# Optimization experiments

Hardware: AMD Instinct MI355X
Metric: run time of the kernel (lower is better)

The kernel has to match this reference:

```python
import jax, jax.numpy as jnp
import numpy as np
from jax.ops import segment_sum, segment_max

N = 400000          # points
V = 100000          # occupied voxels
EPS = 1e-3          # BN eps from norm_cfg
VX, VY, VZ = 0.2, 0.2, 4.0          # voxel_size
X0, Y0, Z0 = 0.0, -40.0, -3.0       # point_cloud_range mins
GX, GY, GZ = 352, 400, 1            # grid dims


def setup_inputs() -> dict:
    key = jax.random.key(0)
    ks = jax.random.split(key, 12)
    # points: xyz uniform inside the point cloud range, 4th channel = intensity
    xyz = jax.random.uniform(ks[0], (N, 3), jnp.float32) \
        * jnp.array([70.4, 80.0, 4.0], jnp.float32) \
        + jnp.array([X0, Y0, Z0], jnp.float32)
    inten = jax.random.uniform(ks[1], (N, 1), jnp.float32)
    features = jnp.concatenate([xyz, inten], axis=1)
    # point -> voxel mapping; guarantee every voxel id occupied so
    # segment_max semantics match torch's unique-voxel reduce exactly
    inv = jnp.concatenate([jnp.arange(V, dtype=jnp.int32),
                           jax.random.randint(ks[2], (N - V,), 0, V, jnp.int32)])
    inv = jax.random.permutation(ks[3], inv)
    # voxel coordinates (batch, z, y, x)
    b = jax.random.randint(ks[4], (V,), 0, 2, jnp.int32)
    z = jnp.zeros((V,), jnp.int32)
    y = jax.random.randint(ks[5], (V,), 0, GY, jnp.int32)
    x = jax.random.randint(ks[6], (V,), 0, GX, jnp.int32)
    coors = jnp.stack([b, z, y, x], axis=1)
    # VFE params: Linear(bias=False) + BN1d(gamma, beta)
    W0 = jax.random.normal(ks[7], (64, 10), jnp.float32) * (1.0 / np.sqrt(10))
    W1 = jax.random.normal(ks[8], (64, 128), jnp.float32) * (1.0 / np.sqrt(128))
    return dict(features=features, W0=W0,
                gamma0=jnp.ones((64,), jnp.float32), beta0=jnp.zeros((64,), jnp.float32),
                W1=W1,
                gamma1=jnp.ones((64,), jnp.float32), beta1=jnp.zeros((64,), jnp.float32),
                inv=inv, coors=coors)


def _bn_relu(x, gamma, beta):
    # BN1d in training mode: biased batch stats over the point dim
    mu = jnp.mean(x, axis=0)
    var = jnp.var(x, axis=0)
    return jax.nn.relu(gamma * (x - mu) * jax.lax.rsqrt(var + EPS) + beta)


def _stats(xyz, inv, coors):
    # cluster-center offset: per-voxel mean of xyz, gathered back
    cnt = segment_sum(jnp.ones((xyz.shape[0],), xyz.dtype), inv, num_segments=V)
    mean = segment_sum(xyz, inv, num_segments=V) / cnt[:, None]
    f_cluster = xyz - mean[inv]
    # voxel-center offset: coors order is (batch, z, y, x)
    cf = coors.astype(xyz.dtype)
    center = jnp.stack([cf[:, 3] * VX + VX / 2 + X0,
                        cf[:, 2] * VY + VY / 2 + Y0,
                        cf[:, 1] * VZ + VZ / 2 + Z0], axis=1)
    f_center = xyz - center[inv]
    return jnp.concatenate([xyz, f_cluster, f_center], axis=1)  # [N, 9]


def reference(features, W0, gamma0, beta0, W1, gamma1, beta1, inv, coors):
    x = jnp.concatenate([_stats(features[:, :3], inv, coors), features[:, 3:]], axis=1)  # [N,10]
    # VFE layer 0
    h0 = _bn_relu(x @ W0.T, gamma0, beta0)                     # [N,64]
    v0 = segment_max(h0, inv, num_segments=V)                  # [V,64]
    x1 = jnp.concatenate([h0, v0[inv]], axis=1)                # [N,128]
    # VFE layer 1
    h1 = _bn_relu(x1 @ W1.T, gamma1, beta1)                    # [N,64]
    voxel_feats = segment_max(h1, inv, num_segments=V)         # [V,64]
    return voxel_feats, coors
```

## Files before the change

### kernel.cpp

```cpp
#include <hip/hip_runtime.h>
#include <hip/hip_bf16.h>

#define NPTS 400000
#define NVOX 100000
#define EPSB 1e-3f
#define NTILE 6250
#define NBLK_SCAN 391
#define GBLK 782

#define OFF_ACC4   0
#define OFF_GRAM   (4*NVOX)
#define OFF_STATS  (OFF_GRAM + 72)
#define OFF_P1     (OFF_STATS + 256)
#define ZERO_FLOATS (OFF_P1 + 4096)
#define OFF_V0     ZERO_FLOATS
#define OFF_Y1M    (OFF_V0 + NVOX*64)
#define OFF_VTMP   (OFF_Y1M + NVOX*64)
#define OFF_BSUM   (OFF_VTMP + NVOX)
#define OFF_VOFF   (OFF_BSUM + 512)
#define OFF_VSTART (OFF_VOFF + NVOX)
#define OFF_ORD    (OFF_VSTART + NVOX + 8)
#define OFF_VS     (OFF_ORD + NPTS)
#define OFF_W0F    (OFF_VS + NPTS)
#define OFF_W1B    (OFF_W0F + 640)
#define OFF_H0T    (OFF_W1B + 4096)

#define XTB_LD 136
#define HT_LD  65

typedef __bf16 bf16x8 __attribute__((ext_vector_type(8)));
typedef float  f32x4  __attribute__((ext_vector_type(4)));

__device__ __forceinline__ float b2f(__hip_bfloat16 h) { return __bfloat162float(h); }
__device__ __forceinline__ float bfbits2f(unsigned short u) {
    return __uint_as_float((unsigned int)u << 16);
}
__device__ __forceinline__ unsigned short bf16u(float f) {
    __hip_bfloat16 h = __float2bfloat16(f);
    return __builtin_bit_cast(unsigned short, h);
}
__device__ __forceinline__ unsigned int fkey(float f) {
    unsigned int u = __float_as_uint(f);
    return (u & 0x80000000u) ? ~u : (u | 0x80000000u);
}
__device__ __forceinline__ float funkey(unsigned int k) {
    unsigned int u = (k & 0x80000000u) ? (k & 0x7FFFFFFFu) : ~k;
    return __uint_as_float(u);
}

__device__ __forceinline__ void compute_x(const __hip_bfloat16* __restrict__ feat,
                                          const float* __restrict__ acc4,
                                          const int* __restrict__ coors,
                                          long i, int v, float* xv) {
    ushort4 f4 = *(const ushort4*)(feat + 4 * i);
    float px = bfbits2f(f4.x), py = bfbits2f(f4.y), pz = bfbits2f(f4.z), it = bfbits2f(f4.w);
    float4 a4 = *(const float4*)&acc4[4 * (long)v];
    float ic = 1.0f / a4.x;
    int4 c4 = *(const int4*)&coors[4 * (long)v];
    xv[0] = px; xv[1] = py; xv[2] = pz;
    xv[3] = px - a4.y * ic; xv[4] = py - a4.z * ic; xv[5] = pz - a4.w * ic;
    xv[6] = px - ((float)c4.w * 0.2f + 0.1f);
    xv[7] = py - ((float)c4.z * 0.2f + 0.1f - 40.0f);
    xv[8] = pz - ((float)c4.y * 4.0f + 2.0f - 3.0f);
    xv[9] = it;
}

__global__ void k_vsum(const __hip_bfloat16* __restrict__ feat,
                       const int* __restrict__ inv,
                       float* __restrict__ acc4,
                       const __hip_bfloat16* __restrict__ W0,
                       const __hip_bfloat16* __restrict__ W1,
                       float* __restrict__ W0f, unsigned short* __restrict__ w1b) {
    if (blockIdx.x == 6250) {
        int t = threadIdx.x;
        for (int j = t; j < 640; j += 256) W0f[j] = b2f(W0[j]);
        for (int f = t; f < 8192; f += 256) {
            int j  = f & 7;
            int l  = (f >> 3) & 63;
            int ks = (f >> 9) & 3;
            int ct = f >> 11;
            int ch = ct * 16 + (l & 15);
            int k  = ks * 32 + ((l >> 4) & 3) * 8 + j;
            w1b[f] = __builtin_bit_cast(unsigned short, W1[ch * 128 + k]);
        }
        return;
    }
    long t = (long)blockIdx.x * 256 + threadIdx.x;
    int pt = (int)(t >> 2);
    int comp = (int)(t & 3);
    float val = (comp == 0) ? 1.0f : b2f(feat[4 * pt + comp - 1]);
    int v = inv[pt];
    atomicAdd(&acc4[(long)v * 4 + comp], val);
}

__global__ void k_scan1(const float* __restrict__ acc4,
                        int* __restrict__ vtmp, int* __restrict__ bsum) {
    __shared__ int sc[256];
    int b = blockIdx.x, t = threadIdx.x;
    int v = b * 256 + t;
    int c = (v < NVOX) ? (int)acc4[4 * (long)v] : 0;
    sc[t] = c;
    __syncthreads();
    int val = c;
    for (int off = 1; off < 256; off <<= 1) {
        int x = (t >= off) ? sc[t - off] : 0;
        __syncthreads();
        val += x; sc[t] = val;
        __syncthreads();
    }
    if (v < NVOX) vtmp[v] = val - c;
    if (t == 255) bsum[b] = val;
}

__global__ void k_scan2(int* __restrict__ bsum) {
    __shared__ int sc[512];
    int t = threadIdx.x;
    int c = (t < NBLK_SCAN) ? bsum[t] : 0;
    sc[t] = c;
    __syncthreads();
    int val = c;
    for (int off = 1; off < 512; off <<= 1) {
        int x = (t >= off) ? sc[t - off] : 0;
        __syncthreads();
        val += x; sc[t] = val;
        __syncthreads();
    }
    if (t < NBLK_SCAN) bsum[t] = val - c;
}

__global__ void k_scan3(const int* __restrict__ vtmp, const int* __restrict__ bsum,
                        int* __restrict__ voff, int* __restrict__ vstart,
                        float* __restrict__ v0, unsigned int* __restrict__ y1m) {
    int v = blockIdx.x * 256 + threadIdx.x;
    if (v < NVOX) {
        int s0 = vtmp[v] + bsum[v >> 8];
        voff[v] = s0;
        vstart[v] = s0;
        int s1;
        if (v + 1 < NVOX) s1 = vtmp[v + 1] + bsum[(v + 1) >> 8];
        else              s1 = NPTS;
        if ((s0 >> 4) != ((s1 - 1) >> 4)) {
            float4 z4 = {0.f, 0.f, 0.f, 0.f};
            float4* pv = (float4*)&v0[(long)v * 64];
            float4* py = (float4*)&y1m[(long)v * 64];
#pragma unroll
            for (int u = 0; u < 16; u++) { pv[u] = z4; py[u] = z4; }
        }
    }
    if (v == 0) vstart[NVOX] = NPTS;
}

__global__ __launch_bounds__(256, 4)
void k_prep(const __hip_bfloat16* __restrict__ feat,
            const int* __restrict__ inv,
            const int* __restrict__ coors,
            const float* __restrict__ acc4,
            int* __restrict__ voff,
            int* __restrict__ ord, int* __restrict__ vsorted,
            float* __restrict__ gram) {
    __shared__ float gs[72];
    int t = threadIdx.x;
    if (t < 72) gs[t] = 0.0f;
    __syncthreads();

    float sx[10], sxx[55];
#pragma unroll
    for (int a = 0; a < 10; a++) sx[a] = 0.0f;
#pragma unroll
    for (int a = 0; a < 55; a++) sxx[a] = 0.0f;

    for (long i = (long)blockIdx.x * 256 + t; i < NPTS; i += (long)GBLK * 256) {
        int v = inv[i];
        float xv[10];
        compute_x(feat, acc4, coors, i, v, xv);
        int idx = 0;
#pragma unroll
        for (int a = 0; a < 10; a++) {
            sx[a] += xv[a];
#pragma unroll
            for (int b = 0; b <= a; b++) sxx[idx++] += xv[a] * xv[b];
        }
        int pos = atomicAdd(&voff[v], 1);
        ord[pos] = (int)i;
        vsorted[pos] = v;
    }

#pragma unroll
    for (int v = 0; v < 65; v++) {
        float s = (v < 10) ? sx[v] : sxx[v - 10];
        for (int m = 32; m >= 1; m >>= 1) s += __shfl_xor(s, m);
        if ((t & 63) == 0) atomicAdd(&gs[v], s);
    }
    __syncthreads();
    if (t < 65) atomicAdd(&gram[t], gs[t]);
}

__global__ __launch_bounds__(256, 8)
void k_h0max(const int* __restrict__ ord, const int* __restrict__ vsorted,
             const int* __restrict__ vstart,
             const __hip_bfloat16* __restrict__ feat,
             const float* __restrict__ acc4, const int* __restrict__ coors,
             const float* __restrict__ W0f, const float* __restrict__ gram,
             const __hip_bfloat16* __restrict__ g0,
             const __hip_bfloat16* __restrict__ be0,
             float* __restrict__ v0, unsigned short* __restrict__ h0t) {
    __shared__ float ht[64 * HT_LD];
    __shared__ int invs[64];
    __shared__ float xvs[640];
    __shared__ float sc0s[64], bi0s[64];
    int t = threadIdx.x, w = t >> 6, l = t & 63;
    int base = blockIdx.x * 64;

    if (w == 0) {
        int i = ord[base + l];
        int v = vsorted[base + l];
        invs[l] = v;
        float xv[10];
        compute_x(feat, acc4, coors, (long)i, v, xv);
#pragma unroll
        for (int k = 0; k < 10; k++) xvs[k * 64 + l] = xv[k];
    } else if (w == 1) {
        int c = l;
        float wr[10];
#pragma unroll
        for (int k = 0; k < 10; k++) wr[k] = W0f[c * 10 + k];
        float sum = 0.0f, sq = 0.0f;
#pragma unroll
        for (int a = 0; a < 10; a++) {
            sum += wr[a] * gram[a];
            float ta = 0.0f;
#pragma unroll
            for (int b = 0; b < 10; b++) {
                int hi = (a >= b) ? a : b, lo = (a >= b) ? b : a;
                ta += wr[b] * gram[10 + hi * (hi + 1) / 2 + lo];
            }
            sq += wr[a] * ta;
        }
        float mu  = sum * (1.0f / NPTS);
        float var = sq * (1.0f / NPTS) - mu * mu;
        float g   = b2f(g0[c]) * rsqrtf(var + EPSB);
        sc0s[c] = g;
        bi0s[c] = b2f(be0[c]) - mu * g;
    }
    __syncthreads();

    float xv[10];
#pragma unroll
    for (int k = 0; k < 10; k++) xv[k] = xvs[k * 64 + l];
    int cw = w * 16;
#pragma unroll
    for (int j = 0; j < 16; j++) {
        int c = cw + j;
        float y = 0.0f;
#pragma unroll
        for (int k = 0; k < 10; k++) y += xv[k] * W0f[c * 10 + k];
        ht[l * HT_LD + c] = fmaxf(sc0s[c] * y + bi0s[c], 0.0f);
    }
    __syncthreads();

#pragma unroll
    for (int u = 0; u < 2; u++) {
        int idx = t + u * 256;
        int pt2 = idx >> 3;
        int c0 = (idx & 7) * 8;
        const float* src = &ht[pt2 * HT_LD + c0];
        float4 a  = *(const float4*)src;
        float4 b4 = *(const float4*)(src + 4);
        uint4 o;
        o.x = (unsigned int)bf16u(a.x)  | ((unsigned int)bf16u(a.y)  << 16);
        o.y = (unsigned int)bf16u(a.z)  | ((unsigned int)bf16u(a.w)  << 16);
        o.z = (unsigned int)bf16u(b4.x) | ((unsigned int)bf16u(b4.y) << 16);
        o.w = (unsigned int)bf16u(b4.z) | ((unsigned int)bf16u(b4.w) << 16);
        *(uint4*)&h0t[(long)(base + pt2) * 64 + c0] = o;
    }

    unsigned int mk = 0u;
#pragma unroll
    for (int j = 0; j < 16; j++) {
        int p = cw + j;
        unsigned int hb = __float_as_uint(ht[p * HT_LD + l]);
        mk = (hb > mk) ? hb : mk;
        if (j == 15 || invs[p + 1] != invs[p]) {
            int vv = invs[p];
            int s0 = vstart[vv], s1 = vstart[vv + 1];
            unsigned int* dst = (unsigned int*)&v0[(long)vv * 64 + l];
            if (s0 >= base + cw && s1 <= base + cw + 16)
                *dst = mk;
            else
                atomicMax(dst, mk);
            mk = 0u;
        }
    }
}

__global__ __launch_bounds__(256, 8)
void k_mfma_stats(const int* __restrict__ vsorted,
                  const int* __restrict__ vstart,
                  const unsigned short* __restrict__ h0t,
                  const unsigned short* __restrict__ w1b,
                  const float* __restrict__ v0,
                  float* __restrict__ P1,
                  unsigned int* __restrict__ y1m) {
    __shared__ union {
        unsigned short xtb[64 * XTB_LD];
        float ht[64 * HT_LD];
    } sm;
    __shared__ int invs[64];
    int t = threadIdx.x, w = t >> 6, l = t & 63;
    int quad = l >> 4, lm = l & 15;
    int base = blockIdx.x * 64;
    if (w == 0) invs[l] = vsorted[base + l];

    bf16x8 bfrag[4];
    const uint4* wf = (const uint4*)w1b;
#pragma unroll
    for (int ks = 0; ks < 4; ks++)
        bfrag[ks] = __builtin_bit_cast(bf16x8, wf[(w * 4 + ks) * 64 + l]);

#pragma unroll
    for (int u = 0; u < 2; u++) {
        int idx = t + u * 256;
        int pt = idx >> 3, c0 = (idx & 7) * 8;
        uint4 d = *(const uint4*)&h0t[(long)(base + pt) * 64 + c0];
        *(uint4*)&sm.xtb[pt * XTB_LD + c0] = d;
    }
    {
        int p = t >> 2, q = t & 3;
        int vv = vsorted[base + p];
        const float4* src = (const float4*)&v0[(long)vv * 64 + q * 16];
#pragma unroll
        for (int u = 0; u < 4; u++) {
            float4 f4 = src[u];
            ushort4 s4 = { bf16u(f4.x), bf16u(f4.y), bf16u(f4.z), bf16u(f4.w) };
            *(ushort4*)&sm.xtb[p * XTB_LD + 64 + q * 16 + 4 * u] = s4;
        }
    }
    __syncthreads();

    f32x4 acc[4];
#pragma unroll
    for (int pg = 0; pg < 4; pg++) acc[pg] = (f32x4){0.f, 0.f, 0.f, 0.f};
#pragma unroll
    for (int ks = 0; ks < 4; ks++) {
#pragma unroll
        for (int pg = 0; pg < 4; pg++) {
            const uint4* ap = (const uint4*)&sm.xtb[(pg * 16 + lm) * XTB_LD + ks * 32 + quad * 8];
            bf16x8 a = __builtin_bit_cast(bf16x8, *ap);
            acc[pg] = __builtin_amdgcn_mfma_f32_16x16x32_bf16(a, bfrag[ks], acc[pg], 0, 0, 0);
        }
    }

    float ssum = 0.0f, ssq = 0.0f;
#pragma unroll
    for (int pg = 0; pg < 4; pg++) {
#pragma unroll
        for (int r = 0; r < 4; r++) {
            float y = acc[pg][r];
            ssum += y; ssq += y * y;
        }
    }
    __syncthreads();

#pragma unroll
    for (int pg = 0; pg < 4; pg++) {
#pragma unroll
        for (int r = 0; r < 4; r++)
            sm.ht[(pg * 16 + quad * 4 + r) * HT_LD + w * 16 + lm] = acc[pg][r];
    }
    __syncthreads();

    unsigned int mk = 0u;
    int cw = w * 16;
#pragma unroll
    for (int j = 0; j < 16; j++) {
        int p = cw + j;
        unsigned int k2 = fkey(sm.ht[p * HT_LD + l]);
        mk = (k2 > mk) ? k2 : mk;
        if (j == 15 || invs[p + 1] != invs[p]) {
            int vv = invs[p];
            int s0 = vstart[vv], s1 = vstart[vv + 1];
            unsigned int* dst = &y1m[(long)vv * 64 + l];
            if (s0 >= base + cw && s1 <= base + cw + 16)
                *dst = mk;
            else
                atomicMax(dst, mk);
            mk = 0u;
        }
    }

    ssum += __shfl_xor(ssum, 16); ssq += __shfl_xor(ssq, 16);
    ssum += __shfl_xor(ssum, 32); ssq += __shfl_xor(ssq, 32);
    if (l < 16) {
        int slot = blockIdx.x & 31;
        atomicAdd(&P1[slot * 128 + w * 16 + lm], ssum);
        atomicAdd(&P1[slot * 128 + 64 + w * 16 + lm], ssq);
    }
}

#define OUTBLK 512
__global__ __launch_bounds__(256)
void k_out(const unsigned int* __restrict__ y1m,
           const float* __restrict__ P1,
           const __hip_bfloat16* __restrict__ gamma,
           const __hip_bfloat16* __restrict__ beta,
           const int* __restrict__ coors,
           float* __restrict__ out) {
    __shared__ float sc1s[64], bi1s[64];
    int t = threadIdx.x;
    if (t < 64) {
        float sum = 0.0f, sq = 0.0f;
        for (int s = 0; s < 32; s++) {
            sum += P1[s*128 + t];
            sq  += P1[s*128 + 64 + t];
        }
        float mu  = sum * (1.0f / NPTS);
        float var = sq * (1.0f / NPTS) - mu * mu;
        float g   = b2f(gamma[t]) * rsqrtf(var + EPSB);
        sc1s[t] = g;
        bi1s[t] = b2f(beta[t]) - mu * g;
    }
    __syncthreads();

    const long n4feat = (long)NVOX * 16;
    const long n4all  = n4feat + NVOX;
    const long nfeat  = (long)NVOX * 64;
    for (long idx = (long)blockIdx.x * 256 + t; idx < n4all; idx += (long)OUTBLK * 256) {
        if (idx < n4feat) {
            uint4 kk = ((const uint4*)y1m)[idx];
            int c0 = (int)((idx * 4) & 63);
            float4 o;
            o.x = fmaxf(sc1s[c0+0] * funkey(kk.x) + bi1s[c0+0], 0.0f);
            o.y = fmaxf(sc1s[c0+1] * funkey(kk.y) + bi1s[c0+1], 0.0f);
            o.z = fmaxf(sc1s[c0+2] * funkey(kk.z) + bi1s[c0+2], 0.0f);
            o.w = fmaxf(sc1s[c0+3] * funkey(kk.w) + bi1s[c0+3], 0.0f);
            ((float4*)out)[idx] = o;
        } else {
            long vi = idx - n4feat;
            int4 c4 = ((const int4*)coors)[vi];
            float4 o;
            o.x = b2f(__float2bfloat16((float)c4.x));
            o.y = b2f(__float2bfloat16((float)c4.y));
            o.z = b2f(__float2bfloat16((float)c4.z));
            o.w = b2f(__float2bfloat16((float)c4.w));
            ((float4*)(out + nfeat))[vi] = o;
        }
    }
}

extern "C" void kernel_launch(void* const* d_in, const int* in_sizes, int n_in,
                              void* d_out, int out_size, void* d_ws, size_t ws_size,
                              hipStream_t stream) {
    const __hip_bfloat16* feat = (const __hip_bfloat16*)d_in[0];
    const __hip_bfloat16* W0   = (const __hip_bfloat16*)d_in[1];
    const __hip_bfloat16* g0   = (const __hip_bfloat16*)d_in[2];
    const __hip_bfloat16* be0  = (const __hip_bfloat16*)d_in[3];
    const __hip_bfloat16* W1   = (const __hip_bfloat16*)d_in[4];
    const __hip_bfloat16* g1   = (const __hip_bfloat16*)d_in[5];
    const __hip_bfloat16* be1  = (const __hip_bfloat16*)d_in[6];
    const int* inv   = (const int*)d_in[7];
    const int* coors = (const int*)d_in[8];
    float* out = (float*)d_out;

    float* ws    = (float*)d_ws;
    float* acc4  = ws + OFF_ACC4;
    float* gram  = ws + OFF_GRAM;
    float* P1    = ws + OFF_P1;
    float* v0    = ws + OFF_V0;
    unsigned int* y1m = (unsigned int*)(ws + OFF_Y1M);
    int* vtmp    = (int*)(ws + OFF_VTMP);
    int* bsum    = (int*)(ws + OFF_BSUM);
    int* voff    = (int*)(ws + OFF_VOFF);
    int* vstart  = (int*)(ws + OFF_VSTART);
    int* ord     = (int*)(ws + OFF_ORD);
    int* vsorted = (int*)(ws + OFF_VS);
    float* W0f   = ws + OFF_W0F;
    unsigned short* w1b = (unsigned short*)(ws + OFF_W1B);
    unsigned short* h0t = (unsigned short*)(ws + OFF_H0T);

    hipMemsetAsync(ws, 0, (size_t)ZERO_FLOATS * sizeof(float), stream);

    k_vsum<<<6251, 256, 0, stream>>>(feat, inv, acc4, W0, W1, W0f, w1b);
    k_scan1<<<NBLK_SCAN, 256, 0, stream>>>(acc4, vtmp, bsum);
    k_scan2<<<1, 512, 0, stream>>>(bsum);
    k_scan3<<<NBLK_SCAN, 256, 0, stream>>>(vtmp, bsum, voff, vstart, v0, y1m);
    k_prep<<<GBLK, 256, 0, stream>>>(feat, inv, coors, acc4, voff, ord, vsorted, gram);
    k_h0max<<<NTILE, 256, 0, stream>>>(ord, vsorted, vstart, feat, acc4, coors,
                                       W0f, gram, g0, be0, v0, h0t);
    k_mfma_stats<<<NTILE, 256, 0, stream>>>(vsorted, vstart, h0t, w1b, v0, P1, y1m);
    k_out<<<OUTBLK, 256, 0, stream>>>(y1m, P1, g1, be1, coors, out);
}
```

Baseline: 265.9 us.

## Fuse layer-0 VFE and layer-1 MFMA kernels, recomputing boundary voxel halos

Merges the h0/segment-max kernel and the MFMA layer-1 kernel into one. Each 64-point tile computes h0 directly into shared memory and keeps per-voxel maxima in an LDS table. For voxels that straddle the tile edge, it recomputes the neighbouring points' h0 so the v0 max is complete locally. This removes the global h0t and v0 buffers, their zeroing, and one launch, in exchange for redundant halo work, LDS atomics, and lower occupancy from a larger shared footprint.

Result: slower. 276.4 us (+3.9%).

```diff
diff --git a/kernel.cpp b/kernel.cpp
--- a/kernel.cpp
+++ b/kernel.cpp
@@ -10,11 +10,9 @@
 
 #define OFF_ACC4   0
 #define OFF_GRAM   (4*NVOX)
-#define OFF_STATS  (OFF_GRAM + 72)
-#define OFF_P1     (OFF_STATS + 256)
+#define OFF_P1     (OFF_GRAM + 128)
 #define ZERO_FLOATS (OFF_P1 + 4096)
-#define OFF_V0     ZERO_FLOATS
-#define OFF_Y1M    (OFF_V0 + NVOX*64)
+#define OFF_Y1M    ZERO_FLOATS
 #define OFF_VTMP   (OFF_Y1M + NVOX*64)
 #define OFF_BSUM   (OFF_VTMP + NVOX)
 #define OFF_VOFF   (OFF_BSUM + 512)
@@ -23,7 +21,6 @@
 #define OFF_VS     (OFF_ORD + NPTS)
 #define OFF_W0F    (OFF_VS + NPTS)
 #define OFF_W1B    (OFF_W0F + 640)
-#define OFF_H0T    (OFF_W1B + 4096)
 
 #define XTB_LD 136
 #define HT_LD  65
@@ -130,7 +127,7 @@
 
 __global__ void k_scan3(const int* __restrict__ vtmp, const int* __restrict__ bsum,
                         int* __restrict__ voff, int* __restrict__ vstart,
-                        float* __restrict__ v0, unsigned int* __restrict__ y1m) {
+                        unsigned int* __restrict__ y1m) {
     int v = blockIdx.x * 256 + threadIdx.x;
     if (v < NVOX) {
         int s0 = vtmp[v] + bsum[v >> 8];
@@ -141,10 +138,9 @@
         else              s1 = NPTS;
         if ((s0 >> 4) != ((s1 - 1) >> 4)) {
             float4 z4 = {0.f, 0.f, 0.f, 0.f};
-            float4* pv = (float4*)&v0[(long)v * 64];
             float4* py = (float4*)&y1m[(long)v * 64];
 #pragma unroll
-            for (int u = 0; u < 16; u++) { pv[u] = z4; py[u] = z4; }
+            for (int u = 0; u < 16; u++) py[u] = z4;
         }
     }
     if (v == 0) vstart[NVOX] = NPTS;
@@ -195,21 +191,35 @@
     if (t < 65) atomicAdd(&gram[t], gs[t]);
 }
 
-__global__ __launch_bounds__(256, 8)
-void k_h0max(const int* __restrict__ ord, const int* __restrict__ vsorted,
+__global__ __launch_bounds__(256, 4)
+void k_fused(const int* __restrict__ ord, const int* __restrict__ vsorted,
              const int* __restrict__ vstart,
              const __hip_bfloat16* __restrict__ feat,
              const float* __restrict__ acc4, const int* __restrict__ coors,
              const float* __restrict__ W0f, const float* __restrict__ gram,
              const __hip_bfloat16* __restrict__ g0,
              const __hip_bfloat16* __restrict__ be0,
-             float* __restrict__ v0, unsigned short* __restrict__ h0t) {
-    __shared__ float ht[64 * HT_LD];
+             const unsigned short* __restrict__ w1b,
+             float* __restrict__ P1, unsigned int* __restrict__ y1m) {
+    __shared__ union {
+        unsigned short xtb[64 * XTB_LD];
+        float ht[64 * HT_LD];
+    } sm;
+    __shared__ unsigned int vms[64 * 65];
+    __shared__ float xvs[640];
     __shared__ int invs[64];
-    __shared__ float xvs[640];
     __shared__ float sc0s[64], bi0s[64];
+    __shared__ int sext[2];
+
     int t = threadIdx.x, w = t >> 6, l = t & 63;
+    int quad = l >> 4, lm = l & 15;
     int base = blockIdx.x * 64;
+
+#pragma unroll
+    for (int u = 0; u < 17; u++) {
+        int idx = t + u * 256;
+        if (idx < 64 * 65) vms[idx] = 0u;
+    }
 
     if (w == 0) {
         int i = ord[base + l];
@@ -219,6 +229,8 @@
         compute_x(feat, acc4, coors, (long)i, v, xv);
 #pragma unroll
         for (int k = 0; k < 10; k++) xvs[k * 64 + l] = xv[k];
+        if (l == 0)  sext[0] = vstart[v];
+        if (l == 63) sext[1] = vstart[v + 1];
     } else if (w == 1) {
         int c = l;
         float wr[10];
@@ -242,74 +254,6 @@
         sc0s[c] = g;
         bi0s[c] = b2f(be0[c]) - mu * g;
     }
-    __syncthreads();
-
-    float xv[10];
-#pragma unroll
-    for (int k = 0; k < 10; k++) xv[k] = xvs[k * 64 + l];
-    int cw = w * 16;
-#pragma unroll
-    for (int j = 0; j < 16; j++) {
-        int c = cw + j;
-        float y = 0.0f;
-#pragma unroll
-        for (int k = 0; k < 10; k++) y += xv[k] * W0f[c * 10 + k];
-        ht[l * HT_LD + c] = fmaxf(sc0s[c] * y + bi0s[c], 0.0f);
-    }
-    __syncthreads();
-
-#pragma unroll
-    for (int u = 0; u < 2; u++) {
-        int idx = t + u * 256;
-        int pt2 = idx >> 3;
-        int c0 = (idx & 7) * 8;
-        const float* src = &ht[pt2 * HT_LD + c0];
-        float4 a  = *(const float4*)src;
-        float4 b4 = *(const float4*)(src + 4);
-        uint4 o;
-        o.x = (unsigned int)bf16u(a.x)  | ((unsigned int)bf16u(a.y)  << 16);
-        o.y = (unsigned int)bf16u(a.z)  | ((unsigned int)bf16u(a.w)  << 16);
-        o.z = (unsigned int)bf16u(b4.x) | ((unsigned int)bf16u(b4.y) << 16);
-        o.w = (unsigned int)bf16u(b4.z) | ((unsigned int)bf16u(b4.w) << 16);
-        *(uint4*)&h0t[(long)(base + pt2) * 64 + c0] = o;
-    }
-
-    unsigned int mk = 0u;
-#pragma unroll
-    for (int j = 0; j < 16; j++) {
-        int p = cw + j;
-        unsigned int hb = __float_as_uint(ht[p * HT_LD + l]);
-        mk = (hb > mk) ? hb : mk;
-        if (j == 15 || invs[p + 1] != invs[p]) {
-            int vv = invs[p];
-            int s0 = vstart[vv], s1 = vstart[vv + 1];
-            unsigned int* dst = (unsigned int*)&v0[(long)vv * 64 + l];
-            if (s0 >= base + cw && s1 <= base + cw + 16)
-                *dst = mk;
-            else
-                atomicMax(dst, mk);
-            mk = 0u;
-        }
-    }
-}
-
-__global__ __launch_bounds__(256, 8)
-void k_mfma_stats(const int* __restrict__ vsorted,
-                  const int* __restrict__ vstart,
-                  const unsigned short* __restrict__ h0t,
-                  const unsigned short* __restrict__ w1b,
-                  const float* __restrict__ v0,
-                  float* __restrict__ P1,
-                  unsigned int* __restrict__ y1m) {
-    __shared__ union {
-        unsigned short xtb[64 * XTB_LD];
-        float ht[64 * HT_LD];
-    } sm;
-    __shared__ int invs[64];
-    int t = threadIdx.x, w = t >> 6, l = t & 63;
-    int quad = l >> 4, lm = l & 15;
-    int base = blockIdx.x * 64;
-    if (w == 0) invs[l] = vsorted[base + l];
 
     bf16x8 bfrag[4];
     const uint4* wf = (const uint4*)w1b;
@@ -317,21 +261,75 @@
     for (int ks = 0; ks < 4; ks++)
         bfrag[ks] = __builtin_bit_cast(bf16x8, wf[(w * 4 + ks) * 64 + l]);
 
-#pragma unroll
-    for (int u = 0; u < 2; u++) {
-        int idx = t + u * 256;
-        int pt = idx >> 3, c0 = (idx & 7) * 8;
-        uint4 d = *(const uint4*)&h0t[(long)(base + pt) * 64 + c0];
-        *(uint4*)&sm.xtb[pt * XTB_LD + c0] = d;
-    }
+    __syncthreads();
+
+    int v_lo = invs[0];
+    int cw = w * 16;
+
+    {
+        float xv[10];
+#pragma unroll
+        for (int k = 0; k < 10; k++) xv[k] = xvs[k * 64 + l];
+        int slot = invs[l] - v_lo;
+#pragma unroll
+        for (int jj = 0; jj < 8; jj++) {
+            int c0 = cw + 2 * jj;
+            float ya = 0.0f, yb = 0.0f;
+#pragma unroll
+            for (int k = 0; k < 10; k++) {
+                ya += xv[k] * W0f[c0 * 10 + k];
+                yb += xv[k] * W0f[(c0 + 1) * 10 + k];
+            }
+            float ha = fmaxf(sc0s[c0] * ya + bi0s[c0], 0.0f);
+            float hb = fmaxf(sc0s[c0 + 1] * yb + bi0s[c0 + 1], 0.0f);
+            unsigned int pk = (unsigned int)bf16u(ha) | ((unsigned int)bf16u(hb) << 16);
+            *(unsigned int*)&sm.xtb[l * XTB_LD + c0] = pk;
+            atomicMax(&vms[slot * 65 + c0],     __float_as_uint(ha));
+            atomicMax(&vms[slot * 65 + c0 + 1], __float_as_uint(hb));
+        }
+    }
+
+    {
+        int s_lo = sext[0], s_hi = sext[1];
+        int L = base - s_lo;
+        int T = s_hi - (base + 64);
+        int v_hi = invs[63];
+        int slot_hi = v_hi - v_lo;
+        for (int j0 = 0; j0 < L + T; j0 += 64) {
+            int j = j0 + l;
+            if (j < L + T) {
+                int lead = (j < L) ? 1 : 0;
+                int g  = lead ? (s_lo + j) : (base + 64 + (j - L));
+                int vv = lead ? v_lo : v_hi;
+                int slot = lead ? 0 : slot_hi;
+                int i = ord[g];
+                float xv[10];
+                compute_x(feat, acc4, coors, (long)i, vv, xv);
+#pragma unroll
+                for (int jj = 0; jj < 16; jj++) {
+                    int c = cw + jj;
+                    float y = 0.0f;
+#pragma unroll
+                    for (int k = 0; k < 10; k++) y += xv[k] * W0f[c * 10 + k];
+                    float h = fmaxf(sc0s[c] * y + bi0s[c], 0.0f);
+                    atomicMax(&vms[slot * 65 + c], __float_as_uint(h));
+                }
+            }
+        }
+    }
+    __syncthreads();
+
     {
         int p = t >> 2, q = t & 3;
-        int vv = vsorted[base + p];
-        const float4* src = (const float4*)&v0[(long)vv * 64 + q * 16];
+        int slot = invs[p] - v_lo;
+        const unsigned int* src = &vms[slot * 65 + q * 16];
 #pragma unroll
         for (int u = 0; u < 4; u++) {
-            float4 f4 = src[u];
-            ushort4 s4 = { bf16u(f4.x), bf16u(f4.y), bf16u(f4.z), bf16u(f4.w) };
+            ushort4 s4;
+            s4.x = bf16u(__uint_as_float(src[4 * u + 0]));
+            s4.y = bf16u(__uint_as_float(src[4 * u + 1]));
+            s4.z = bf16u(__uint_as_float(src[4 * u + 2]));
+            s4.w = bf16u(__uint_as_float(src[4 * u + 3]));
             *(ushort4*)&sm.xtb[p * XTB_LD + 64 + q * 16 + 4 * u] = s4;
         }
     }
@@ -370,7 +368,6 @@
     __syncthreads();
 
     unsigned int mk = 0u;
-    int cw = w * 16;
 #pragma unroll
     for (int j = 0; j < 16; j++) {
         int p = cw + j;
@@ -465,7 +462,6 @@
     float* acc4  = ws + OFF_ACC4;
     float* gram  = ws + OFF_GRAM;
     float* P1    = ws + OFF_P1;
-    float* v0    = ws + OFF_V0;
     unsigned int* y1m = (unsigned int*)(ws + OFF_Y1M);
     int* vtmp    = (int*)(ws + OFF_VTMP);
     int* bsum    = (int*)(ws + OFF_BSUM);
@@ -475,17 +471,15 @@
     int* vsorted = (int*)(ws + OFF_VS);
     float* W0f   = ws + OFF_W0F;
     unsigned short* w1b = (unsigned short*)(ws + OFF_W1B);
-    unsigned short* h0t = (unsigned short*)(ws + OFF_H0T);
 
     hipMemsetAsync(ws, 0, (size_t)ZERO_FLOATS * sizeof(float), stream);
 
     k_vsum<<<6251, 256, 0, stream>>>(feat, inv, acc4, W0, W1, W0f, w1b);
     k_scan1<<<NBLK_SCAN, 256, 0, stream>>>(acc4, vtmp, bsum);
     k_scan2<<<1, 512, 0, stream>>>(bsum);
-    k_scan3<<<NBLK_SCAN, 256, 0, stream>>>(vtmp, bsum, voff, vstart, v0, y1m);
+    k_scan3<<<NBLK_SCAN, 256, 0, stream>>>(vtmp, bsum, voff, vstart, y1m);
     k_prep<<<GBLK, 256, 0, stream>>>(feat, inv, coors, acc4, voff, ord, vsorted, gram);
-    k_h0max<<<NTILE, 256, 0, stream>>>(ord, vsorted, vstart, feat, acc4, coors,
-                                       W0f, gram, g0, be0, v0, h0t);
-    k_mfma_stats<<<NTILE, 256, 0, stream>>>(vsorted, vstart, h0t, w1b, v0, P1, y1m);
+    k_fused<<<NTILE, 256, 0, stream>>>(ord, vsorted, vstart, feat, acc4, coors,
+                                       W0f, gram, g0, be0, w1b, P1, y1m);
     k_out<<<OUTBLK, 256, 0, stream>>>(y1m, P1, g1, be1, coors, out);
 }
```
